# Performance work log

Hardware: AMD Instinct MI355X
Metric: run time of the kernel (lower is better)

## Reference

```python
import jax, jax.numpy as jnp
import numpy as np

N, E, CIN, COUT = 100000, 1600000, 64, 128
EPS = 1e-5  # torch BatchNorm default


def setup_inputs() -> dict:
    key = jax.random.key(0)
    ks = jax.random.split(key, 16)
    s = 0.1
    x = jax.random.normal(ks[0], (N, CIN), jnp.float32)
    src = jax.random.randint(ks[1], (E,), 0, N, dtype=jnp.int32)
    dst = jax.random.randint(ks[2], (E,), 0, N, dtype=jnp.int32)
    edge_index = jnp.stack([src, dst])  # [2, E]
    return {
        "x": x,
        "edge_index": edge_index,
        # conv0: GraphConv(CIN -> COUT)
        "W_root0": jax.random.normal(ks[3], (COUT, CIN), jnp.float32) * s,
        "W_nbr0": jax.random.normal(ks[4], (COUT, CIN), jnp.float32) * s,
        "b0": jnp.zeros((COUT,), jnp.float32),
        # bn0
        "g0": jnp.ones((COUT,), jnp.float32),
        "be0": jnp.zeros((COUT,), jnp.float32),
        # conv1: GraphConv(COUT -> COUT)
        "W_root1": jax.random.normal(ks[5], (COUT, COUT), jnp.float32) * s,
        "W_nbr1": jax.random.normal(ks[6], (COUT, COUT), jnp.float32) * s,
        "b1": jnp.zeros((COUT,), jnp.float32),
        # bn1
        "g1": jnp.ones((COUT,), jnp.float32),
        "be1": jnp.zeros((COUT,), jnp.float32),
        # residual 1x1 conv (Conv1d(CIN, COUT, 1))
        "Wlin": jax.random.normal(ks[7], (COUT, CIN), jnp.float32) * s,
        "blin": jnp.zeros((COUT,), jnp.float32),
    }


def graph_conv(x, src, dst, W_root, W_nbr, b):
    # PyG GraphConv: out_i = W_root x_i + W_nbr * sum_{j: (j->i) in E} x_j + b
    agg = jax.ops.segment_sum(x[src], dst, num_segments=N)  # scatter-add over edges
    return x @ W_root.T + agg @ W_nbr.T + b


def batch_norm(x, gamma, beta):
    # training-mode BatchNorm over the node dimension (biased variance)
    mu = jnp.mean(x, axis=0)
    var = jnp.mean(jnp.square(x - mu), axis=0)
    return (x - mu) * jax.lax.rsqrt(var + EPS) * gamma + beta


def reference(x, edge_index, W_root0, W_nbr0, b0, g0, be0,
              W_root1, W_nbr1, b1, g1, be1, Wlin, blin):
    src, dst = edge_index[0], edge_index[1]
    y = batch_norm(graph_conv(x, src, dst, W_root0, W_nbr0, b0), g0, be0)
    y = jax.nn.relu(y)
    y = batch_norm(graph_conv(y, src, dst, W_root1, W_nbr1, b1), g1, be1)
    out = y + (x @ Wlin.T + blin)  # 1x1 Conv1d residual projection
    return jax.nn.relu(out)
```

## Files before the change

kernel.cpp:

```cpp
#include <hip/hip_runtime.h>
#include <stdint.h>


#define CIN 64
#define COUT 128
#define BN_EPS 1e-5f
#define CURPAD 32
#define PCPAD 32
#define SPAD 32
#define PSH 10
#define PNODES (1 << PSH)
#define MAXP 128

typedef unsigned short u16;
typedef short short8 __attribute__((ext_vector_type(8)));
typedef float f32x4 __attribute__((ext_vector_type(4)));

__device__ __forceinline__ float bf2f(u16 u) {
    union { unsigned int i; float f; } v; v.i = ((unsigned int)u) << 16; return v.f;
}
__device__ __forceinline__ u16 f2bf(float f) {
    union { float f; unsigned int i; } v; v.f = f;
    unsigned int r = v.i + 0x7fffu + ((v.i >> 16) & 1u);
    return (u16)(r >> 16);
}
__device__ __forceinline__ float lo16(unsigned int w) { return bf2f((u16)(w & 0xffffu)); }
__device__ __forceinline__ float hi16(unsigned int w) { return bf2f((u16)(w >> 16)); }

template<bool BF> __device__ __forceinline__ float ldf(const void* p, long i) {
    if (BF) return bf2f(((const u16*)p)[i]);
    return ((const float*)p)[i];
}
template<bool BF> __device__ __forceinline__ short8 ld8(const void* p, long i) {
    if (BF) return *(const short8*)((const u16*)p + i);
    const float* f = (const float*)p + i;
    short8 r;
#pragma unroll
    for (int j = 0; j < 8; ++j) r[j] = (short)f2bf(f[j]);
    return r;
}

__global__ void k_detect(const unsigned int* __restrict__ x, int* __restrict__ flag) {
    int lane = threadIdx.x;
    int cnt = 0;
#pragma unroll
    for (int i = 0; i < 8; ++i) {
        unsigned int w = x[lane * 8 + i];
        unsigned int e0 = (w >> 7) & 0xFFu, e1 = (w >> 23) & 0xFFu;
        cnt += (e0 >= 0x60u && e0 <= 0x8Eu);
        cnt += (e1 >= 0x60u && e1 <= 0x8Eu);
    }
    for (int o = 32; o; o >>= 1) cnt += __shfl_down(cnt, o);
    if (lane == 0) *flag = (cnt > 850) ? 1 : 0;
}

__global__ __launch_bounds__(256) void k_phist(const int* __restrict__ dst,
                                               int* __restrict__ pcount, int E, int np) {
    __shared__ int h[MAXP];
    for (int i = threadIdx.x; i < np; i += 256) h[i] = 0;
    __syncthreads();
    int stride = gridDim.x * 256;
    for (int e = blockIdx.x * 256 + threadIdx.x; e < E; e += stride)
        atomicAdd(&h[dst[e] >> PSH], 1);
    __syncthreads();
    for (int i = threadIdx.x; i < np; i += 256)
        if (h[i]) atomicAdd(&pcount[i * PCPAD], h[i]);
}

__global__ void k_pscan(const int* __restrict__ pcount, int* __restrict__ pstart,
                        int* __restrict__ pcursor, int np, int E) {
    __shared__ int s[MAXP];
    int t = threadIdx.x;
    int v = (t < np) ? pcount[t * PCPAD] : 0;
    s[t] = v; __syncthreads();
    for (int o = 1; o < MAXP; o <<= 1) {
        int u = (t >= o) ? s[t - o] : 0;
        __syncthreads(); s[t] += u; __syncthreads();
    }
    if (t < np) {
        int ex = s[t] - v;
        pstart[t] = ex;
        pcursor[t * CURPAD] = ex;
    }
    if (t == 0) pstart[np] = E;
}

__global__ __launch_bounds__(256) void k_pfill(const int* __restrict__ src,
        const int* __restrict__ dst, int* __restrict__ pcursor,
        unsigned int* __restrict__ barr, int E, int np) {
    __shared__ int cnt[MAXP], gb[MAXP], loc[MAXP];
    int tid = threadIdx.x;
    int base = blockIdx.x * 4096;
    for (int i = tid; i < np; i += 256) { cnt[i] = 0; loc[i] = 0; }
    __syncthreads();
    int pk[16]; unsigned int rec[16];
#pragma unroll
    for (int k = 0; k < 16; ++k) {
        int e = base + k * 256 + tid;
        if (e < E) {
            int d = dst[e];
            pk[k] = d >> PSH;
            rec[k] = ((unsigned int)(d & (PNODES - 1)) << 20) | (unsigned int)src[e];
            atomicAdd(&cnt[pk[k]], 1);
        } else pk[k] = -1;
    }
    __syncthreads();
    for (int i = tid; i < np; i += 256)
        if (cnt[i]) gb[i] = atomicAdd(&pcursor[i * CURPAD], cnt[i]);
    __syncthreads();
#pragma unroll
    for (int k = 0; k < 16; ++k) {
        if (pk[k] >= 0) {
            int off = atomicAdd(&loc[pk[k]], 1);
            barr[gb[pk[k]] + off] = rec[k];
        }
    }
}

__global__ __launch_bounds__(256) void k_psort(const unsigned int* __restrict__ barr,
        const int* __restrict__ pstart, int* __restrict__ csr,
        int* __restrict__ row_start, int n, int np, int E) {
    __shared__ int hist[PNODES], curs[PNODES], tsum[256];
    int tid = threadIdx.x;
    int p = blockIdx.x;
    int e0 = pstart[p], e1 = pstart[p + 1];
    int node0 = p << PSH;
#pragma unroll
    for (int j = 0; j < PNODES / 256; ++j) hist[tid + j * 256] = 0;
    __syncthreads();
    for (int t = e0 + tid; t < e1; t += 256)
        atomicAdd(&hist[barr[t] >> 20], 1);
    __syncthreads();
    int s0 = hist[tid * 4], s1 = hist[tid * 4 + 1], s2 = hist[tid * 4 + 2], s3 = hist[tid * 4 + 3];
    int sum4 = s0 + s1 + s2 + s3;
    tsum[tid] = sum4; __syncthreads();
    for (int o = 1; o < 256; o <<= 1) {
        int u = (tid >= o) ? tsum[tid - o] : 0;
        __syncthreads(); tsum[tid] += u; __syncthreads();
    }
    int bexc = tsum[tid] - sum4;
    int off0 = bexc, off1 = bexc + s0, off2 = off1 + s1, off3 = off2 + s2;
    curs[tid * 4] = off0; curs[tid * 4 + 1] = off1;
    curs[tid * 4 + 2] = off2; curs[tid * 4 + 3] = off3;
    int nd = node0 + tid * 4;
    if (nd < n)     row_start[nd]     = e0 + off0;
    if (nd + 1 < n) row_start[nd + 1] = e0 + off1;
    if (nd + 2 < n) row_start[nd + 2] = e0 + off2;
    if (nd + 3 < n) row_start[nd + 3] = e0 + off3;
    if (p == np - 1 && tid == 0) row_start[n] = E;
    __syncthreads();
    for (int t = e0 + tid; t < e1; t += 256) {
        unsigned int rec = barr[t];
        int pos = atomicAdd(&curs[rec >> 20], 1);
        csr[e0 + pos] = (int)(rec & 0xFFFFF);
    }
}

template<bool BF>
__device__ __forceinline__ void agg0_impl(const void* x, const int* rs, const int* csr,
                                          u16* agg, int n) {
    int i = blockIdx.x * 4 + (threadIdx.x >> 6);
    if (i >= n) return;
    int lane = threadIdx.x & 63;
    int b = rs[i], e = rs[i + 1];
    if (BF) {
        int slot = lane >> 3, cp = lane & 7;
        float acc[8] = {0.f, 0.f, 0.f, 0.f, 0.f, 0.f, 0.f, 0.f};
        int t = b + slot;
        for (; t + 8 < e; t += 16) {
            int j0 = csr[t], j1 = csr[t + 8];
            uint4 w0 = *((const uint4*)((const unsigned int*)x + (long)j0 * 32) + cp);
            uint4 w1 = *((const uint4*)((const unsigned int*)x + (long)j1 * 32) + cp);
            acc[0] += lo16(w0.x); acc[1] += hi16(w0.x);
            acc[2] += lo16(w0.y); acc[3] += hi16(w0.y);
            acc[4] += lo16(w0.z); acc[5] += hi16(w0.z);
            acc[6] += lo16(w0.w); acc[7] += hi16(w0.w);
            acc[0] += lo16(w1.x); acc[1] += hi16(w1.x);
            acc[2] += lo16(w1.y); acc[3] += hi16(w1.y);
            acc[4] += lo16(w1.z); acc[5] += hi16(w1.z);
            acc[6] += lo16(w1.w); acc[7] += hi16(w1.w);
        }
        if (t < e) {
            int j0 = csr[t];
            uint4 w0 = *((const uint4*)((const unsigned int*)x + (long)j0 * 32) + cp);
            acc[0] += lo16(w0.x); acc[1] += hi16(w0.x);
            acc[2] += lo16(w0.y); acc[3] += hi16(w0.y);
            acc[4] += lo16(w0.z); acc[5] += hi16(w0.z);
            acc[6] += lo16(w0.w); acc[7] += hi16(w0.w);
        }
#pragma unroll
        for (int k = 0; k < 8; ++k) {
            acc[k] += __shfl_xor(acc[k], 8);
            acc[k] += __shfl_xor(acc[k], 16);
            acc[k] += __shfl_xor(acc[k], 32);
        }
        if (slot == 0) {
            uint4 o;
            o.x = (unsigned int)f2bf(acc[0]) | ((unsigned int)f2bf(acc[1]) << 16);
            o.y = (unsigned int)f2bf(acc[2]) | ((unsigned int)f2bf(acc[3]) << 16);
            o.z = (unsigned int)f2bf(acc[4]) | ((unsigned int)f2bf(acc[5]) << 16);
            o.w = (unsigned int)f2bf(acc[6]) | ((unsigned int)f2bf(acc[7]) << 16);
            *((uint4*)((unsigned int*)agg + (long)i * 32) + cp) = o;
        }
    } else {
        int slot = lane >> 4, cp = lane & 15;
        float acc[4] = {0.f, 0.f, 0.f, 0.f};
        int t = b + slot;
        for (; t + 4 < e; t += 8) {
            int j0 = csr[t], j1 = csr[t + 4];
            float4 w0 = *((const float4*)((const float*)x + (long)j0 * 64) + cp);
            float4 w1 = *((const float4*)((const float*)x + (long)j1 * 64) + cp);
            acc[0] += w0.x + w1.x; acc[1] += w0.y + w1.y;
            acc[2] += w0.z + w1.z; acc[3] += w0.w + w1.w;
        }
        if (t < e) {
            int j0 = csr[t];
            float4 w0 = *((const float4*)((const float*)x + (long)j0 * 64) + cp);
            acc[0] += w0.x; acc[1] += w0.y; acc[2] += w0.z; acc[3] += w0.w;
        }
#pragma unroll
        for (int k = 0; k < 4; ++k) {
            acc[k] += __shfl_xor(acc[k], 16);
            acc[k] += __shfl_xor(acc[k], 32);
        }
        if (slot == 0) {
            unsigned int o0 = (unsigned int)f2bf(acc[0]) | ((unsigned int)f2bf(acc[1]) << 16);
            unsigned int o1 = (unsigned int)f2bf(acc[2]) | ((unsigned int)f2bf(acc[3]) << 16);
            uint2 o; o.x = o0; o.y = o1;
            *((uint2*)((unsigned int*)agg + (long)i * 32) + cp) = o;
        }
    }
}

__global__ __launch_bounds__(256) void k_agg0(const int* __restrict__ flag,
        const void* x, const int* __restrict__ rs, const int* __restrict__ csr,
        u16* __restrict__ agg, int n) {
    if (*flag) agg0_impl<true >(x, rs, csr, agg, n);
    else       agg0_impl<false>(x, rs, csr, agg, n);
}

__global__ __launch_bounds__(256) void k_y0p(unsigned int* __restrict__ y0,
        const float* __restrict__ sc, const float* __restrict__ sh, long nq) {
    long idx = (long)blockIdx.x * 256 + threadIdx.x;
    int colq = threadIdx.x & 15;
    float s8[8], h8[8];
#pragma unroll
    for (int j = 0; j < 8; ++j) { s8[j] = sc[colq * 8 + j]; h8[j] = sh[colq * 8 + j]; }
    long stride = (long)gridDim.x * 256;
    uint4* p = (uint4*)y0;
    for (; idx < nq; idx += stride) {
        uint4 w = p[idx];
        unsigned int r[4] = {w.x, w.y, w.z, w.w};
        uint4 o;
        unsigned int* po = (unsigned int*)&o;
#pragma unroll
        for (int d = 0; d < 4; ++d) {
            float a = fmaxf(lo16(r[d]) * s8[2 * d]     + h8[2 * d],     0.f);
            float b = fmaxf(hi16(r[d]) * s8[2 * d + 1] + h8[2 * d + 1], 0.f);
            po[d] = (unsigned int)f2bf(a) | ((unsigned int)f2bf(b) << 16);
        }
        p[idx] = o;
    }
}

__global__ __launch_bounds__(256) void k_agg1(const u16* __restrict__ y0p,
        const int* __restrict__ rs, const int* __restrict__ csr,
        u16* __restrict__ agg, int n) {
    int i = blockIdx.x * 4 + (threadIdx.x >> 6);
    if (i >= n) return;
    int lane = threadIdx.x & 63;
    int slot = lane >> 4, cp = lane & 15;
    const unsigned int* y32 = (const unsigned int*)y0p;
    int b = rs[i], e = rs[i + 1];
    float acc[8] = {0.f, 0.f, 0.f, 0.f, 0.f, 0.f, 0.f, 0.f};
    int t = b + slot;
    for (; t + 4 < e; t += 8) {
        int j0 = csr[t], j1 = csr[t + 4];
        uint4 w0 = *((const uint4*)(y32 + (long)j0 * 64) + cp);
        uint4 w1 = *((const uint4*)(y32 + (long)j1 * 64) + cp);
        acc[0] += lo16(w0.x); acc[1] += hi16(w0.x);
        acc[2] += lo16(w0.y); acc[3] += hi16(w0.y);
        acc[4] += lo16(w0.z); acc[5] += hi16(w0.z);
        acc[6] += lo16(w0.w); acc[7] += hi16(w0.w);
        acc[0] += lo16(w1.x); acc[1] += hi16(w1.x);
        acc[2] += lo16(w1.y); acc[3] += hi16(w1.y);
        acc[4] += lo16(w1.z); acc[5] += hi16(w1.z);
        acc[6] += lo16(w1.w); acc[7] += hi16(w1.w);
    }
    if (t < e) {
        int j0 = csr[t];
        uint4 w0 = *((const uint4*)(y32 + (long)j0 * 64) + cp);
        acc[0] += lo16(w0.x); acc[1] += hi16(w0.x);
        acc[2] += lo16(w0.y); acc[3] += hi16(w0.y);
        acc[4] += lo16(w0.z); acc[5] += hi16(w0.z);
        acc[6] += lo16(w0.w); acc[7] += hi16(w0.w);
    }
#pragma unroll
    for (int k = 0; k < 8; ++k) {
        acc[k] += __shfl_xor(acc[k], 16);
        acc[k] += __shfl_xor(acc[k], 32);
    }
    if (slot == 0) {
        uint4 o;
        o.x = (unsigned int)f2bf(acc[0]) | ((unsigned int)f2bf(acc[1]) << 16);
        o.y = (unsigned int)f2bf(acc[2]) | ((unsigned int)f2bf(acc[3]) << 16);
        o.z = (unsigned int)f2bf(acc[4]) | ((unsigned int)f2bf(acc[5]) << 16);
        o.w = (unsigned int)f2bf(acc[6]) | ((unsigned int)f2bf(acc[7]) << 16);
        *((uint4*)((unsigned int*)agg + (long)i * 64) + cp) = o;
    }
}

template<bool BF>
__device__ __forceinline__ void gemm0_impl(const void* x, const u16* agg,
                                           const void* Wr, const void* Wn,
                                           u16* y0, float* sumP, float* sqP,
                                           int n, int nch, u16* lds) {
    const int ST = 130;
    int tid = threadIdx.x;
    int wave = tid >> 6, lane = tid & 63, lr = lane & 15, q = lane >> 4;

    short8 wf[2][4];
#pragma unroll
    for (int i = 0; i < 2; ++i) {
        int c = (2 * wave + i) * 16 + lr;
#pragma unroll
        for (int ks = 0; ks < 4; ++ks) {
            const void* W = (ks < 2) ? Wr : Wn;
            wf[i][ks] = ld8<BF>(W, (long)c * CIN + (ks & 1) * 32 + q * 8);
        }
    }

    const int rowb = tid >> 3, wb = tid & 7;
    const int rowf = tid >> 4, wfc = tid & 15;
    short8 rbx[2]; float4 rfx[4]; short8 rag[2];

    auto regload = [&](long chunk0) {
        if (BF) {
#pragma unroll
            for (int i = 0; i < 2; ++i) {
                long rg = chunk0 + rowb + i * 32; if (rg > n - 1) rg = n - 1;
                rbx[i] = *(const short8*)((const u16*)x + rg * CIN + wb * 8);
            }
        } else {
#pragma unroll
            for (int i = 0; i < 4; ++i) {
                long rg = chunk0 + rowf + i * 16; if (rg > n - 1) rg = n - 1;
                rfx[i] = *(const float4*)((const float*)x + rg * CIN + wfc * 4);
            }
        }
#pragma unroll
        for (int i = 0; i < 2; ++i) {
            long rg = chunk0 + rowb + i * 32; if (rg > n - 1) rg = n - 1;
            rag[i] = *(const short8*)(agg + rg * CIN + wb * 8);
        }
    };

    float st[2] = {0.f, 0.f}, sq[2] = {0.f, 0.f};
    int ch = blockIdx.x;
    if (ch < nch) regload((long)ch * 64);
    for (; ch < nch; ch += gridDim.x) {
        long chunk0 = (long)ch * 64;
        __syncthreads();
        if (BF) {
#pragma unroll
            for (int i = 0; i < 2; ++i)
                *(short8*)(lds + (rowb + i * 32) * ST + wb * 8) = rbx[i];
        } else {
#pragma unroll
            for (int i = 0; i < 4; ++i) {
                u16* d = lds + (rowf + i * 16) * ST + wfc * 4;
                d[0] = f2bf(rfx[i].x); d[1] = f2bf(rfx[i].y);
                d[2] = f2bf(rfx[i].z); d[3] = f2bf(rfx[i].w);
            }
        }
#pragma unroll
        for (int i = 0; i < 2; ++i)
            *(short8*)(lds + (rowb + i * 32) * ST + 64 + wb * 8) = rag[i];
        __syncthreads();
        long nxt = (long)ch + gridDim.x;
        if (nxt < nch) regload(nxt * 64);

#pragma unroll
        for (int t = 0; t < 4; ++t) {
            short8 a[4];
#pragma unroll
            for (int ks = 0; ks < 4; ++ks)
                a[ks] = *(const short8*)(lds + (t * 16 + lr) * ST + ks * 32 + q * 8);
#pragma unroll
            for (int i = 0; i < 2; ++i) {
                f32x4 acc = {0.f, 0.f, 0.f, 0.f};
#pragma unroll
                for (int ks = 0; ks < 4; ++ks)
                    acc = __builtin_amdgcn_mfma_f32_16x16x32_bf16(a[ks], wf[i][ks], acc, 0, 0, 0);
                int c = (2 * wave + i) * 16 + lr;
#pragma unroll
                for (int r = 0; r < 4; ++r) {
                    long row = chunk0 + t * 16 + q * 4 + r;
                    if (row < n) {
                        y0[row * COUT + c] = f2bf(acc[r]);
                        st[i] += acc[r]; sq[i] += acc[r] * acc[r];
                    }
                }
            }
        }
    }
#pragma unroll
    for (int i = 0; i < 2; ++i) {
        st[i] += __shfl_xor(st[i], 16); st[i] += __shfl_xor(st[i], 32);
        sq[i] += __shfl_xor(sq[i], 16); sq[i] += __shfl_xor(sq[i], 32);
    }
    if (q == 0) {
#pragma unroll
        for (int i = 0; i < 2; ++i) {
            int c = (2 * wave + i) * 16 + lr;
            atomicAdd(&sumP[c * SPAD], st[i]);
            atomicAdd(&sqP[c * SPAD], sq[i]);
        }
    }
}

__global__ __launch_bounds__(256) void k_gemm0(const int* __restrict__ flag,
        const void* x, const u16* __restrict__ agg, const void* Wr, const void* Wn,
        u16* __restrict__ y0, float* __restrict__ sumP, float* __restrict__ sqP,
        int n, int nch) {
    __shared__ u16 lds[64 * 130];
    if (*flag) gemm0_impl<true >(x, agg, Wr, Wn, y0, sumP, sqP, n, nch, lds);
    else       gemm0_impl<false>(x, agg, Wr, Wn, y0, sumP, sqP, n, nch, lds);
}

template<bool BF>
__device__ __forceinline__ void gemm1_impl(const u16* y0p, const u16* agg,
                                           const void* Wr, const void* Wn,
                                           u16* y1, float* sumP, float* sqP,
                                           int n, int nch, u16* lds) {
    const int ST = 258;
    int tid = threadIdx.x;
    int wave = tid >> 6, lane = tid & 63, lr = lane & 15, q = lane >> 4;

    short8 wf[2][8];
#pragma unroll
    for (int i = 0; i < 2; ++i) {
        int c = (2 * wave + i) * 16 + lr;
#pragma unroll
        for (int ks = 0; ks < 8; ++ks) {
            const void* W = (ks < 4) ? Wr : Wn;
            wf[i][ks] = ld8<BF>(W, (long)c * COUT + (ks & 3) * 32 + q * 8);
        }
    }

    const int rowy = tid >> 4, wy = tid & 15;
    short8 ry[4], rag[4];
    auto regload = [&](long chunk0) {
#pragma unroll
        for (int i = 0; i < 4; ++i) {
            long rg = chunk0 + rowy + i * 16; if (rg > n - 1) rg = n - 1;
            ry[i]  = *(const short8*)(y0p + rg * COUT + wy * 8);
            rag[i] = *(const short8*)(agg + rg * COUT + wy * 8);
        }
    };

    float st[2] = {0.f, 0.f}, sq[2] = {0.f, 0.f};
    int ch = blockIdx.x;
    if (ch < nch) regload((long)ch * 64);
    for (; ch < nch; ch += gridDim.x) {
        long chunk0 = (long)ch * 64;
        __syncthreads();
#pragma unroll
        for (int i = 0; i < 4; ++i) {
            *(short8*)(lds + (rowy + i * 16) * ST + wy * 8) = ry[i];
            *(short8*)(lds + (rowy + i * 16) * ST + 128 + wy * 8) = rag[i];
        }
        __syncthreads();
        long nxt = (long)ch + gridDim.x;
        if (nxt < nch) regload(nxt * 64);

#pragma unroll
        for (int t = 0; t < 4; ++t) {
            short8 a[8];
#pragma unroll
            for (int ks = 0; ks < 8; ++ks)
                a[ks] = *(const short8*)(lds + (t * 16 + lr) * ST + ks * 32 + q * 8);
#pragma unroll
            for (int i = 0; i < 2; ++i) {
                f32x4 acc = {0.f, 0.f, 0.f, 0.f};
#pragma unroll
                for (int ks = 0; ks < 8; ++ks)
                    acc = __builtin_amdgcn_mfma_f32_16x16x32_bf16(a[ks], wf[i][ks], acc, 0, 0, 0);
                int c = (2 * wave + i) * 16 + lr;
#pragma unroll
                for (int r = 0; r < 4; ++r) {
                    long row = chunk0 + t * 16 + q * 4 + r;
                    if (row < n) {
                        y1[row * COUT + c] = f2bf(acc[r]);
                        st[i] += acc[r]; sq[i] += acc[r] * acc[r];
                    }
                }
            }
        }
    }
#pragma unroll
    for (int i = 0; i < 2; ++i) {
        st[i] += __shfl_xor(st[i], 16); st[i] += __shfl_xor(st[i], 32);
        sq[i] += __shfl_xor(sq[i], 16); sq[i] += __shfl_xor(sq[i], 32);
    }
    if (q == 0) {
#pragma unroll
        for (int i = 0; i < 2; ++i) {
            int c = (2 * wave + i) * 16 + lr;
            atomicAdd(&sumP[c * SPAD], st[i]);
            atomicAdd(&sqP[c * SPAD], sq[i]);
        }
    }
}

__global__ __launch_bounds__(256) void k_gemm1(const int* __restrict__ flag,
        const u16* __restrict__ y0p, const u16* __restrict__ agg,
        const void* Wr, const void* Wn,
        u16* y1_bf , u16* y1_ws,
        float* __restrict__ sumP, float* __restrict__ sqP, int n, int nch) {
    __shared__ u16 lds[64 * 258];
    u16* y1 = *flag ? y1_bf : y1_ws;
    if (*flag) gemm1_impl<true >(y0p, agg, Wr, Wn, y1, sumP, sqP, n, nch, lds);
    else       gemm1_impl<false>(y0p, agg, Wr, Wn, y1, sumP, sqP, n, nch, lds);
}

__global__ void k_bnfin(const int* __restrict__ flag,
                        const float* __restrict__ sumP, const float* __restrict__ sqP,
                        const void* g, const void* be,
                        float* __restrict__ scale, float* __restrict__ shift, int n) {
    int c = threadIdx.x;
    bool bf = (*flag != 0);
    float inv = 1.f / (float)n;
    float mu = sumP[c * SPAD] * inv;
    float var = fmaxf(sqP[c * SPAD] * inv - mu * mu, 0.f);
    float gv = bf ? bf2f(((const u16*)g)[c]) : ((const float*)g)[c];
    float bv = bf ? bf2f(((const u16*)be)[c]) : ((const float*)be)[c];
    float sc = gv * rsqrtf(var + BN_EPS);
    scale[c] = sc;
    shift[c] = bv - mu * sc;
}

template<bool BF>
__device__ __forceinline__ void final_impl(const void* x, const u16* y1,
                                           const void* Wlin, const void* blin,
                                           const float* sc, const float* sh,
                                           void* out, int n, int nch, u16* lds) {
    const int ST = 194;
    int tid = threadIdx.x;
    int wave = tid >> 6, lane = tid & 63, lr = lane & 15, q = lane >> 4;

    short8 wf[2][2];
    float blc[2], scc[2], shc[2];
#pragma unroll
    for (int i = 0; i < 2; ++i) {
        int c = (2 * wave + i) * 16 + lr;
#pragma unroll
        for (int ks = 0; ks < 2; ++ks)
            wf[i][ks] = ld8<BF>(Wlin, (long)c * CIN + ks * 32 + q * 8);
        blc[i] = ldf<BF>(blin, c);
        scc[i] = sc[c]; shc[i] = sh[c];
    }

    const int rowb = tid >> 3, wb = tid & 7;
    const int rowf = tid >> 4, wfc = tid & 15;
    const int rowy = tid >> 4, wy = tid & 15;
    short8 rbx[2]; float4 rfx[4]; short8 ry[4];

    auto regload = [&](long chunk0) {
        if (BF) {
#pragma unroll
            for (int i = 0; i < 2; ++i) {
                long rg = chunk0 + rowb + i * 32; if (rg > n - 1) rg = n - 1;
                rbx[i] = *(const short8*)((const u16*)x + rg * CIN + wb * 8);
            }
        } else {
#pragma unroll
            for (int i = 0; i < 4; ++i) {
                long rg = chunk0 + rowf + i * 16; if (rg > n - 1) rg = n - 1;
                rfx[i] = *(const float4*)((const float*)x + rg * CIN + wfc * 4);
            }
        }
#pragma unroll
        for (int i = 0; i < 4; ++i) {
            long rg = chunk0 + rowy + i * 16; if (rg > n - 1) rg = n - 1;
            ry[i] = *(const short8*)(y1 + rg * COUT + wy * 8);
        }
    };

    int ch = blockIdx.x;
    if (ch < nch) regload((long)ch * 64);
    for (; ch < nch; ch += gridDim.x) {
        long chunk0 = (long)ch * 64;
        __syncthreads();
        if (BF) {
#pragma unroll
            for (int i = 0; i < 2; ++i)
                *(short8*)(lds + (rowb + i * 32) * ST + wb * 8) = rbx[i];
        } else {
#pragma unroll
            for (int i = 0; i < 4; ++i) {
                u16* d = lds + (rowf + i * 16) * ST + wfc * 4;
                d[0] = f2bf(rfx[i].x); d[1] = f2bf(rfx[i].y);
                d[2] = f2bf(rfx[i].z); d[3] = f2bf(rfx[i].w);
            }
        }
#pragma unroll
        for (int i = 0; i < 4; ++i)
            *(short8*)(lds + (rowy + i * 16) * ST + 64 + wy * 8) = ry[i];
        __syncthreads();
        long nxt = (long)ch + gridDim.x;
        if (nxt < nch) regload(nxt * 64);

#pragma unroll
        for (int t = 0; t < 4; ++t) {
            short8 a[2];
#pragma unroll
            for (int ks = 0; ks < 2; ++ks)
                a[ks] = *(const short8*)(lds + (t * 16 + lr) * ST + ks * 32 + q * 8);
#pragma unroll
            for (int i = 0; i < 2; ++i) {
                f32x4 acc = {0.f, 0.f, 0.f, 0.f};
                acc = __builtin_amdgcn_mfma_f32_16x16x32_bf16(a[0], wf[i][0], acc, 0, 0, 0);
                acc = __builtin_amdgcn_mfma_f32_16x16x32_bf16(a[1], wf[i][1], acc, 0, 0, 0);
                int c = (2 * wave + i) * 16 + lr;
#pragma unroll
                for (int r = 0; r < 4; ++r) {
                    long row = chunk0 + t * 16 + q * 4 + r;
                    if (row < n) {
                        float yv = bf2f(lds[(t * 16 + q * 4 + r) * ST + 64 + c]);
                        float v = acc[r] + blc[i] + yv * scc[i] + shc[i];
                        v = fmaxf(v, 0.f);
                        if (BF) ((u16*)out)[row * COUT + c] = f2bf(v);
                        else    ((float*)out)[row * COUT + c] = v;
                    }
                }
            }
        }
    }
}

__global__ __launch_bounds__(256) void k_final(const int* __restrict__ flag,
        const void* x, const void* Wlin, const void* blin,
        const u16* y1_bf , const u16* y1_ws,
        const float* __restrict__ sc, const float* __restrict__ sh,
        void* out, int n, int nch) {
    __shared__ u16 lds[64 * 194];
    const u16* y1 = *flag ? y1_bf : y1_ws;
    if (*flag) final_impl<true >(x, y1, Wlin, blin, sc, sh, out, n, nch, lds);
    else       final_impl<false>(x, y1, Wlin, blin, sc, sh, out, n, nch, lds);
}

extern "C" void kernel_launch(void* const* d_in, const int* in_sizes, int n_in,
                              void* d_out, int out_size, void* d_ws, size_t ws_size,
                              hipStream_t stream) {
    (void)n_in; (void)out_size; (void)ws_size;
    const void* x    = d_in[0];
    const int*  ei   = (const int*)d_in[1];
    const void* Wr0  = d_in[2];
    const void* Wn0  = d_in[3];
    const void* g0   = d_in[5];
    const void* be0  = d_in[6];
    const void* Wr1  = d_in[7];
    const void* Wn1  = d_in[8];
    const void* g1   = d_in[10];
    const void* be1  = d_in[11];
    const void* Wlin = d_in[12];
    const void* blin = d_in[13];

    const int N = in_sizes[0] / CIN;
    const int E = in_sizes[1] / 2;
    const int* src = ei;
    const int* dst = ei + E;
    const int NP = (N + PNODES - 1) >> PSH;

    char* base = (char*)d_ws;
    size_t off = 0;
    auto carve = [&](size_t bytes) -> void* {
        void* p = base + off;
        off = (off + bytes + 255) & ~(size_t)255;
        return p;
    };
    int*   flag      = (int*)carve(256);
    int*   pcount    = (int*)carve(MAXP * PCPAD * sizeof(int));
    int*   pstart    = (int*)carve((MAXP + 1) * sizeof(int));
    int*   pcursor   = (int*)carve(MAXP * CURPAD * sizeof(int));
    float* statsP    = (float*)carve(4 * 128 * SPAD * sizeof(float));
    float* scsh      = (float*)carve(512 * sizeof(float));
    int*   row_start = (int*)carve((size_t)(N + 1) * sizeof(int));
    unsigned int* barr = (unsigned int*)carve((size_t)E * sizeof(int));
    int*   csr       = (int*)carve((size_t)E * sizeof(int));
    u16*   aggu      = (u16*)carve((size_t)N * COUT * sizeof(u16));
    u16*   y0        = (u16*)carve((size_t)N * COUT * sizeof(u16));
    u16*   y1_ws     = (u16*)carve((size_t)N * COUT * sizeof(u16));

    float* sum0P = statsP;
    float* sq0P  = statsP + 128 * SPAD;
    float* sum1P = statsP + 256 * SPAD;
    float* sq1P  = statsP + 384 * SPAD;

    hipMemsetAsync(pcount, 0, MAXP * PCPAD * sizeof(int), stream);
    hipMemsetAsync(statsP, 0, 4 * 128 * SPAD * sizeof(float), stream);

    const int nwb = (N + 3) / 4;
    const int nch = (N + 63) / 64;
    const int ntl = (E + 4095) / 4096;
    const int G   = nch < 1024 ? nch : 1024;
    const long nq = (long)N * 16;
    int g2 = (int)((nq + 255) / 256); if (g2 > 2048) g2 = 2048;

    k_detect<<<1, 64, 0, stream>>>((const unsigned int*)x, flag);

    k_phist<<<256, 256, 0, stream>>>(dst, pcount, E, NP);
    k_pscan<<<1, MAXP, 0, stream>>>(pcount, pstart, pcursor, NP, E);
    k_pfill<<<ntl, 256, 0, stream>>>(src, dst, pcursor, barr, E, NP);
    k_psort<<<NP, 256, 0, stream>>>(barr, pstart, csr, row_start, N, NP, E);

    k_agg0 <<<nwb, 256, 0, stream>>>(flag, x, row_start, csr, aggu, N);
    k_gemm0<<<G, 256, 0, stream>>>(flag, x, aggu, Wr0, Wn0, y0,
                                   sum0P, sq0P, N, nch);
    k_bnfin<<<1, 128, 0, stream>>>(flag, sum0P, sq0P, g0, be0,
                                   scsh, scsh + 128, N);

    k_y0p<<<g2, 256, 0, stream>>>((unsigned int*)y0, scsh, scsh + 128, nq);

    k_agg1 <<<nwb, 256, 0, stream>>>(y0, row_start, csr, aggu, N);
    k_gemm1<<<G, 256, 0, stream>>>(flag, y0, aggu, Wr1, Wn1,
                                   (u16*)d_out, y1_ws, sum1P, sq1P, N, nch);
    k_bnfin<<<1, 128, 0, stream>>>(flag, sum1P, sq1P, g1, be1,
                                   scsh + 256, scsh + 384, N);

    k_final<<<G, 256, 0, stream>>>(flag, x, Wlin, blin,
                                   (const u16*)d_out, y1_ws,
                                   scsh + 256, scsh + 384, d_out, N, nch);
}
```

Baseline: 397.0 us.

## Shrink GEMM row chunks, finer partitions, narrower bf16 gather, deeper unroll

Several changes land together. Node partitions for the CSR sort shrink from 1024 to 256 nodes, so there are more blocks and one histogram bin per thread. The bf16 layer-0 gather now uses 16 lanes of 8-byte loads with four edges in flight, and both aggregation loops unroll to four edges per iteration. The GEMM and final kernels process 32-row chunks instead of 64, with a larger grid cap and occupancy launch bounds, aiming for more waves per CU and less LDS per block at the cost of more loop iterations and redundant weight-fragment setup.

```diff
diff --git a/kernel.cpp b/kernel.cpp
--- a/kernel.cpp
+++ b/kernel.cpp
@@ -8,9 +8,9 @@
 #define CURPAD 32
 #define PCPAD 32
 #define SPAD 32
-#define PSH 10
+#define PSH 8
 #define PNODES (1 << PSH)
-#define MAXP 128
+#define MAXP 512
 
 typedef unsigned short u16;
 typedef short short8 __attribute__((ext_vector_type(8)));
@@ -125,28 +125,21 @@
     int p = blockIdx.x;
     int e0 = pstart[p], e1 = pstart[p + 1];
     int node0 = p << PSH;
-#pragma unroll
-    for (int j = 0; j < PNODES / 256; ++j) hist[tid + j * 256] = 0;
+    hist[tid] = 0;
     __syncthreads();
     for (int t = e0 + tid; t < e1; t += 256)
         atomicAdd(&hist[barr[t] >> 20], 1);
     __syncthreads();
-    int s0 = hist[tid * 4], s1 = hist[tid * 4 + 1], s2 = hist[tid * 4 + 2], s3 = hist[tid * 4 + 3];
-    int sum4 = s0 + s1 + s2 + s3;
-    tsum[tid] = sum4; __syncthreads();
+    int v = hist[tid];
+    tsum[tid] = v; __syncthreads();
     for (int o = 1; o < 256; o <<= 1) {
         int u = (tid >= o) ? tsum[tid - o] : 0;
         __syncthreads(); tsum[tid] += u; __syncthreads();
     }
-    int bexc = tsum[tid] - sum4;
-    int off0 = bexc, off1 = bexc + s0, off2 = off1 + s1, off3 = off2 + s2;
-    curs[tid * 4] = off0; curs[tid * 4 + 1] = off1;
-    curs[tid * 4 + 2] = off2; curs[tid * 4 + 3] = off3;
-    int nd = node0 + tid * 4;
-    if (nd < n)     row_start[nd]     = e0 + off0;
-    if (nd + 1 < n) row_start[nd + 1] = e0 + off1;
-    if (nd + 2 < n) row_start[nd + 2] = e0 + off2;
-    if (nd + 3 < n) row_start[nd + 3] = e0 + off3;
+    int ex = tsum[tid] - v;
+    curs[tid] = ex;
+    int nd = node0 + tid;
+    if (nd < n) row_start[nd] = e0 + ex;
     if (p == np - 1 && tid == 0) row_start[n] = E;
     __syncthreads();
     for (int t = e0 + tid; t < e1; t += 256) {
@@ -162,58 +155,55 @@
     int i = blockIdx.x * 4 + (threadIdx.x >> 6);
     if (i >= n) return;
     int lane = threadIdx.x & 63;
+    int slot = lane >> 4, cp = lane & 15;
     int b = rs[i], e = rs[i + 1];
     if (BF) {
-        int slot = lane >> 3, cp = lane & 7;
-        float acc[8] = {0.f, 0.f, 0.f, 0.f, 0.f, 0.f, 0.f, 0.f};
+        const unsigned int* x32 = (const unsigned int*)x;
+        float acc[4] = {0.f, 0.f, 0.f, 0.f};
         int t = b + slot;
-        for (; t + 8 < e; t += 16) {
-            int j0 = csr[t], j1 = csr[t + 8];
-            uint4 w0 = *((const uint4*)((const unsigned int*)x + (long)j0 * 32) + cp);
-            uint4 w1 = *((const uint4*)((const unsigned int*)x + (long)j1 * 32) + cp);
+        for (; t + 12 < e; t += 16) {
+            int j0 = csr[t], j1 = csr[t + 4], j2 = csr[t + 8], j3 = csr[t + 12];
+            uint2 w0 = *((const uint2*)(x32 + (long)j0 * 32) + cp);
+            uint2 w1 = *((const uint2*)(x32 + (long)j1 * 32) + cp);
+            uint2 w2 = *((const uint2*)(x32 + (long)j2 * 32) + cp);
+            uint2 w3 = *((const uint2*)(x32 + (long)j3 * 32) + cp);
+            acc[0] += lo16(w0.x) + lo16(w1.x); acc[1] += hi16(w0.x) + hi16(w1.x);
+            acc[2] += lo16(w0.y) + lo16(w1.y); acc[3] += hi16(w0.y) + hi16(w1.y);
+            acc[0] += lo16(w2.x) + lo16(w3.x); acc[1] += hi16(w2.x) + hi16(w3.x);
+            acc[2] += lo16(w2.y) + lo16(w3.y); acc[3] += hi16(w2.y) + hi16(w3.y);
+        }
+        for (; t < e; t += 4) {
+            int j0 = csr[t];
+            uint2 w0 = *((const uint2*)(x32 + (long)j0 * 32) + cp);
             acc[0] += lo16(w0.x); acc[1] += hi16(w0.x);
             acc[2] += lo16(w0.y); acc[3] += hi16(w0.y);
-            acc[4] += lo16(w0.z); acc[5] += hi16(w0.z);
-            acc[6] += lo16(w0.w); acc[7] += hi16(w0.w);
-            acc[0] += lo16(w1.x); acc[1] += hi16(w1.x);
-            acc[2] += lo16(w1.y); acc[3] += hi16(w1.y);
-            acc[4] += lo16(w1.z); acc[5] += hi16(w1.z);
-            acc[6] += lo16(w1.w); acc[7] += hi16(w1.w);
-        }
-        if (t < e) {
-            int j0 = csr[t];
-            uint4 w0 = *((const uint4*)((const unsigned int*)x + (long)j0 * 32) + cp);
-            acc[0] += lo16(w0.x); acc[1] += hi16(w0.x);
-            acc[2] += lo16(w0.y); acc[3] += hi16(w0.y);
-            acc[4] += lo16(w0.z); acc[5] += hi16(w0.z);
-            acc[6] += lo16(w0.w); acc[7] += hi16(w0.w);
-        }
-#pragma unroll
-        for (int k = 0; k < 8; ++k) {
-            acc[k] += __shfl_xor(acc[k], 8);
+        }
+#pragma unroll
+        for (int k = 0; k < 4; ++k) {
             acc[k] += __shfl_xor(acc[k], 16);
             acc[k] += __shfl_xor(acc[k], 32);
         }
         if (slot == 0) {
-            uint4 o;
+            uint2 o;
             o.x = (unsigned int)f2bf(acc[0]) | ((unsigned int)f2bf(acc[1]) << 16);
             o.y = (unsigned int)f2bf(acc[2]) | ((unsigned int)f2bf(acc[3]) << 16);
-            o.z = (unsigned int)f2bf(acc[4]) | ((unsigned int)f2bf(acc[5]) << 16);
-            o.w = (unsigned int)f2bf(acc[6]) | ((unsigned int)f2bf(acc[7]) << 16);
-            *((uint4*)((unsigned int*)agg + (long)i * 32) + cp) = o;
+            *((uint2*)((unsigned int*)agg + (long)i * 32) + cp) = o;
         }
     } else {
-        int slot = lane >> 4, cp = lane & 15;
         float acc[4] = {0.f, 0.f, 0.f, 0.f};
         int t = b + slot;
-        for (; t + 4 < e; t += 8) {
-            int j0 = csr[t], j1 = csr[t + 4];
+        for (; t + 12 < e; t += 16) {
+            int j0 = csr[t], j1 = csr[t + 4], j2 = csr[t + 8], j3 = csr[t + 12];
             float4 w0 = *((const float4*)((const float*)x + (long)j0 * 64) + cp);
             float4 w1 = *((const float4*)((const float*)x + (long)j1 * 64) + cp);
-            acc[0] += w0.x + w1.x; acc[1] += w0.y + w1.y;
-            acc[2] += w0.z + w1.z; acc[3] += w0.w + w1.w;
-        }
-        if (t < e) {
+            float4 w2 = *((const float4*)((const float*)x + (long)j2 * 64) + cp);
+            float4 w3 = *((const float4*)((const float*)x + (long)j3 * 64) + cp);
+            acc[0] += (w0.x + w1.x) + (w2.x + w3.x);
+            acc[1] += (w0.y + w1.y) + (w2.y + w3.y);
+            acc[2] += (w0.z + w1.z) + (w2.z + w3.z);
+            acc[3] += (w0.w + w1.w) + (w2.w + w3.w);
+        }
+        for (; t < e; t += 4) {
             int j0 = csr[t];
             float4 w0 = *((const float4*)((const float*)x + (long)j0 * 64) + cp);
             acc[0] += w0.x; acc[1] += w0.y; acc[2] += w0.z; acc[3] += w0.w;
@@ -224,9 +214,9 @@
             acc[k] += __shfl_xor(acc[k], 32);
         }
         if (slot == 0) {
-            unsigned int o0 = (unsigned int)f2bf(acc[0]) | ((unsigned int)f2bf(acc[1]) << 16);
-            unsigned int o1 = (unsigned int)f2bf(acc[2]) | ((unsigned int)f2bf(acc[3]) << 16);
-            uint2 o; o.x = o0; o.y = o1;
+            uint2 o;
+            o.x = (unsigned int)f2bf(acc[0]) | ((unsigned int)f2bf(acc[1]) << 16);
+            o.y = (unsigned int)f2bf(acc[2]) | ((unsigned int)f2bf(acc[3]) << 16);
             *((uint2*)((unsigned int*)agg + (long)i * 32) + cp) = o;
         }
     }
@@ -274,20 +264,22 @@
     int b = rs[i], e = rs[i + 1];
     float acc[8] = {0.f, 0.f, 0.f, 0.f, 0.f, 0.f, 0.f, 0.f};
     int t = b + slot;
-    for (; t + 4 < e; t += 8) {
-        int j0 = csr[t], j1 = csr[t + 4];
+    for (; t + 12 < e; t += 16) {
+        int j0 = csr[t], j1 = csr[t + 4], j2 = csr[t + 8], j3 = csr[t + 12];
         uint4 w0 = *((const uint4*)(y32 + (long)j0 * 64) + cp);
         uint4 w1 = *((const uint4*)(y32 + (long)j1 * 64) + cp);
-        acc[0] += lo16(w0.x); acc[1] += hi16(w0.x);
-        acc[2] += lo16(w0.y); acc[3] += hi16(w0.y);
-        acc[4] += lo16(w0.z); acc[5] += hi16(w0.z);
-        acc[6] += lo16(w0.w); acc[7] += hi16(w0.w);
-        acc[0] += lo16(w1.x); acc[1] += hi16(w1.x);
-        acc[2] += lo16(w1.y); acc[3] += hi16(w1.y);
-        acc[4] += lo16(w1.z); acc[5] += hi16(w1.z);
-        acc[6] += lo16(w1.w); acc[7] += hi16(w1.w);
-    }
-    if (t < e) {
+        uint4 w2 = *((const uint4*)(y32 + (long)j2 * 64) + cp);
+        uint4 w3 = *((const uint4*)(y32 + (long)j3 * 64) + cp);
+        acc[0] += lo16(w0.x) + lo16(w1.x); acc[1] += hi16(w0.x) + hi16(w1.x);
+        acc[2] += lo16(w0.y) + lo16(w1.y); acc[3] += hi16(w0.y) + hi16(w1.y);
+        acc[4] += lo16(w0.z) + lo16(w1.z); acc[5] += hi16(w0.z) + hi16(w1.z);
+        acc[6] += lo16(w0.w) + lo16(w1.w); acc[7] += hi16(w0.w) + hi16(w1.w);
+        acc[0] += lo16(w2.x) + lo16(w3.x); acc[1] += hi16(w2.x) + hi16(w3.x);
+        acc[2] += lo16(w2.y) + lo16(w3.y); acc[3] += hi16(w2.y) + hi16(w3.y);
+        acc[4] += lo16(w2.z) + lo16(w3.z); acc[5] += hi16(w2.z) + hi16(w3.z);
+        acc[6] += lo16(w2.w) + lo16(w3.w); acc[7] += hi16(w2.w) + hi16(w3.w);
+    }
+    for (; t < e; t += 4) {
         int j0 = csr[t];
         uint4 w0 = *((const uint4*)(y32 + (long)j0 * 64) + cp);
         acc[0] += lo16(w0.x); acc[1] += hi16(w0.x);
@@ -332,56 +324,46 @@
 
     const int rowb = tid >> 3, wb = tid & 7;
     const int rowf = tid >> 4, wfc = tid & 15;
-    short8 rbx[2]; float4 rfx[4]; short8 rag[2];
+    short8 rbx1; float4 rfx[2]; short8 rag1;
 
     auto regload = [&](long chunk0) {
         if (BF) {
+            long rg = chunk0 + rowb; if (rg > n - 1) rg = n - 1;
+            rbx1 = *(const short8*)((const u16*)x + rg * CIN + wb * 8);
+        } else {
 #pragma unroll
             for (int i = 0; i < 2; ++i) {
-                long rg = chunk0 + rowb + i * 32; if (rg > n - 1) rg = n - 1;
-                rbx[i] = *(const short8*)((const u16*)x + rg * CIN + wb * 8);
-            }
-        } else {
-#pragma unroll
-            for (int i = 0; i < 4; ++i) {
                 long rg = chunk0 + rowf + i * 16; if (rg > n - 1) rg = n - 1;
                 rfx[i] = *(const float4*)((const float*)x + rg * CIN + wfc * 4);
             }
         }
-#pragma unroll
-        for (int i = 0; i < 2; ++i) {
-            long rg = chunk0 + rowb + i * 32; if (rg > n - 1) rg = n - 1;
-            rag[i] = *(const short8*)(agg + rg * CIN + wb * 8);
-        }
+        long rg = chunk0 + rowb; if (rg > n - 1) rg = n - 1;
+        rag1 = *(const short8*)(agg + rg * CIN + wb * 8);
     };
 
     float st[2] = {0.f, 0.f}, sq[2] = {0.f, 0.f};
     int ch = blockIdx.x;
-    if (ch < nch) regload((long)ch * 64);
+    if (ch < nch) regload((long)ch * 32);
     for (; ch < nch; ch += gridDim.x) {
-        long chunk0 = (long)ch * 64;
+        long chunk0 = (long)ch * 32;
         __syncthreads();
         if (BF) {
-#pragma unroll
-            for (int i = 0; i < 2; ++i)
-                *(short8*)(lds + (rowb + i * 32) * ST + wb * 8) = rbx[i];
+            *(short8*)(lds + rowb * ST + wb * 8) = rbx1;
         } else {
 #pragma unroll
-            for (int i = 0; i < 4; ++i) {
+            for (int i = 0; i < 2; ++i) {
                 u16* d = lds + (rowf + i * 16) * ST + wfc * 4;
                 d[0] = f2bf(rfx[i].x); d[1] = f2bf(rfx[i].y);
                 d[2] = f2bf(rfx[i].z); d[3] = f2bf(rfx[i].w);
             }
         }
-#pragma unroll
-        for (int i = 0; i < 2; ++i)
-            *(short8*)(lds + (rowb + i * 32) * ST + 64 + wb * 8) = rag[i];
+        *(short8*)(lds + rowb * ST + 64 + wb * 8) = rag1;
         __syncthreads();
         long nxt = (long)ch + gridDim.x;
-        if (nxt < nch) regload(nxt * 64);
-
-#pragma unroll
-        for (int t = 0; t < 4; ++t) {
+        if (nxt < nch) regload(nxt * 32);
+
+#pragma unroll
+        for (int t = 0; t < 2; ++t) {
             short8 a[4];
 #pragma unroll
             for (int ks = 0; ks < 4; ++ks)
@@ -419,11 +401,11 @@
     }
 }
 
-__global__ __launch_bounds__(256) void k_gemm0(const int* __restrict__ flag,
+__global__ __launch_bounds__(256, 6) void k_gemm0(const int* __restrict__ flag,
         const void* x, const u16* __restrict__ agg, const void* Wr, const void* Wn,
         u16* __restrict__ y0, float* __restrict__ sumP, float* __restrict__ sqP,
         int n, int nch) {
-    __shared__ u16 lds[64 * 130];
+    __shared__ u16 lds[32 * 130];
     if (*flag) gemm0_impl<true >(x, agg, Wr, Wn, y0, sumP, sqP, n, nch, lds);
     else       gemm0_impl<false>(x, agg, Wr, Wn, y0, sumP, sqP, n, nch, lds);
 }
@@ -449,10 +431,10 @@
     }
 
     const int rowy = tid >> 4, wy = tid & 15;
-    short8 ry[4], rag[4];
+    short8 ry[2], rag[2];
     auto regload = [&](long chunk0) {
 #pragma unroll
-        for (int i = 0; i < 4; ++i) {
+        for (int i = 0; i < 2; ++i) {
             long rg = chunk0 + rowy + i * 16; if (rg > n - 1) rg = n - 1;
             ry[i]  = *(const short8*)(y0p + rg * COUT + wy * 8);
             rag[i] = *(const short8*)(agg + rg * COUT + wy * 8);
@@ -461,21 +443,21 @@
 
     float st[2] = {0.f, 0.f}, sq[2] = {0.f, 0.f};
     int ch = blockIdx.x;
-    if (ch < nch) regload((long)ch * 64);
+    if (ch < nch) regload((long)ch * 32);
     for (; ch < nch; ch += gridDim.x) {
-        long chunk0 = (long)ch * 64;
+        long chunk0 = (long)ch * 32;
         __syncthreads();
 #pragma unroll
-        for (int i = 0; i < 4; ++i) {
+        for (int i = 0; i < 2; ++i) {
             *(short8*)(lds + (rowy + i * 16) * ST + wy * 8) = ry[i];
             *(short8*)(lds + (rowy + i * 16) * ST + 128 + wy * 8) = rag[i];
         }
         __syncthreads();
         long nxt = (long)ch + gridDim.x;
-        if (nxt < nch) regload(nxt * 64);
-
-#pragma unroll
-        for (int t = 0; t < 4; ++t) {
+        if (nxt < nch) regload(nxt * 32);
+
+#pragma unroll
+        for (int t = 0; t < 2; ++t) {
             short8 a[8];
 #pragma unroll
             for (int ks = 0; ks < 8; ++ks)
@@ -513,12 +495,12 @@
     }
 }
 
-__global__ __launch_bounds__(256) void k_gemm1(const int* __restrict__ flag,
+__global__ __launch_bounds__(256, 5) void k_gemm1(const int* __restrict__ flag,
         const u16* __restrict__ y0p, const u16* __restrict__ agg,
         const void* Wr, const void* Wn,
         u16* y1_bf , u16* y1_ws,
         float* __restrict__ sumP, float* __restrict__ sqP, int n, int nch) {
-    __shared__ u16 lds[64 * 258];
+    __shared__ u16 lds[32 * 258];
     u16* y1 = *flag ? y1_bf : y1_ws;
     if (*flag) gemm1_impl<true >(y0p, agg, Wr, Wn, y1, sumP, sqP, n, nch, lds);
     else       gemm1_impl<false>(y0p, agg, Wr, Wn, y1, sumP, sqP, n, nch, lds);
@@ -564,55 +546,50 @@
     const int rowb = tid >> 3, wb = tid & 7;
     const int rowf = tid >> 4, wfc = tid & 15;
     const int rowy = tid >> 4, wy = tid & 15;
-    short8 rbx[2]; float4 rfx[4]; short8 ry[4];
+    short8 rbx1; float4 rfx[2]; short8 ry[2];
 
     auto regload = [&](long chunk0) {
         if (BF) {
+            long rg = chunk0 + rowb; if (rg > n - 1) rg = n - 1;
+            rbx1 = *(const short8*)((const u16*)x + rg * CIN + wb * 8);
+        } else {
 #pragma unroll
             for (int i = 0; i < 2; ++i) {
-                long rg = chunk0 + rowb + i * 32; if (rg > n - 1) rg = n - 1;
-                rbx[i] = *(const short8*)((const u16*)x + rg * CIN + wb * 8);
-            }
-        } else {
-#pragma unroll
-            for (int i = 0; i < 4; ++i) {
                 long rg = chunk0 + rowf + i * 16; if (rg > n - 1) rg = n - 1;
                 rfx[i] = *(const float4*)((const float*)x + rg * CIN + wfc * 4);
             }
         }
 #pragma unroll
-        for (int i = 0; i < 4; ++i) {
+        for (int i = 0; i < 2; ++i) {
             long rg = chunk0 + rowy + i * 16; if (rg > n - 1) rg = n - 1;
             ry[i] = *(const short8*)(y1 + rg * COUT + wy * 8);
         }
     };
 
     int ch = blockIdx.x;
-    if (ch < nch) regload((long)ch * 64);
+    if (ch < nch) regload((long)ch * 32);
     for (; ch < nch; ch += gridDim.x) {
-        long chunk0 = (long)ch * 64;
+        long chunk0 = (long)ch * 32;
         __syncthreads();
         if (BF) {
-#pragma unroll
-            for (int i = 0; i < 2; ++i)
-                *(short8*)(lds + (rowb + i * 32) * ST + wb * 8) = rbx[i];
+            *(short8*)(lds + rowb * ST + wb * 8) = rbx1;
         } else {
 #pragma unroll
-            for (int i = 0; i < 4; ++i) {
+            for (int i = 0; i < 2; ++i) {
                 u16* d = lds + (rowf + i * 16) * ST + wfc * 4;
                 d[0] = f2bf(rfx[i].x); d[1] = f2bf(rfx[i].y);
                 d[2] = f2bf(rfx[i].z); d[3] = f2bf(rfx[i].w);
             }
         }
 #pragma unroll
-        for (int i = 0; i < 4; ++i)
+        for (int i = 0; i < 2; ++i)
             *(short8*)(lds + (rowy + i * 16) * ST + 64 + wy * 8) = ry[i];
         __syncthreads();
         long nxt = (long)ch + gridDim.x;
-        if (nxt < nch) regload(nxt * 64);
-
-#pragma unroll
-        for (int t = 0; t < 4; ++t) {
+        if (nxt < nch) regload(nxt * 32);
+
+#pragma unroll
+        for (int t = 0; t < 2; ++t) {
             short8 a[2];
 #pragma unroll
             for (int ks = 0; ks < 2; ++ks)
@@ -639,12 +616,12 @@
     }
 }
 
-__global__ __launch_bounds__(256) void k_final(const int* __restrict__ flag,
+__global__ __launch_bounds__(256, 6) void k_final(const int* __restrict__ flag,
         const void* x, const void* Wlin, const void* blin,
         const u16* y1_bf , const u16* y1_ws,
         const float* __restrict__ sc, const float* __restrict__ sh,
         void* out, int n, int nch) {
-    __shared__ u16 lds[64 * 194];
+    __shared__ u16 lds[32 * 194];
     const u16* y1 = *flag ? y1_bf : y1_ws;
     if (*flag) final_impl<true >(x, y1, Wlin, blin, sc, sh, out, n, nch, lds);
     else       final_impl<false>(x, y1, Wlin, blin, sc, sh, out, n, nch, lds);
@@ -702,9 +679,9 @@
     hipMemsetAsync(statsP, 0, 4 * 128 * SPAD * sizeof(float), stream);
 
     const int nwb = (N + 3) / 4;
-    const int nch = (N + 63) / 64;
+    const int nch = (N + 31) / 32;
     const int ntl = (E + 4095) / 4096;
-    const int G   = nch < 1024 ? nch : 1024;
+    const int G   = nch < 2048 ? nch : 2048;
     const long nq = (long)N * 16;
     int g2 = (int)((nq + 255) / 256); if (g2 > 2048) g2 = 2048;
 
```

Measured after the change: 574.1 us. 1.45x slower.
